# Performance work log

Hardware: AMD Instinct MI355X
Metric: run time of the kernel (lower is better)

Reference implementation:

```python
import jax, jax.numpy as jnp
import numpy as np

IOU_POS = 0.6
IOU_NEG = 0.45
BOX_W, CLS_W, INT_W = 1.0, 1.0, 0.5
ALPHA, GAMMA = 0.25, 2.0
BETA = 1.0 / 9.0
EPS = 1e-6


def setup_inputs() -> dict:
    key = jax.random.key(0)
    ks = jax.random.split(key, 8)
    B, N, M, C = 8, 131072, 48, 8
    cls_logits = jax.random.normal(ks[0], (B, N, 1), jnp.float32)
    box_preds = jax.random.normal(ks[1], (B, N, 6), jnp.float32) * 0.1
    intention_logits = jax.random.normal(ks[2], (B, N, C), jnp.float32)
    # anchors: 256x256 BEV grid over 100x100m, 2 orientations -> 131072 anchors
    side = int(np.sqrt(N // 2))
    xs = jnp.linspace(0.0, 100.0, side)
    gx, gy = jnp.meshgrid(xs, xs, indexing='ij')
    base = jnp.stack([gx.ravel(), gy.ravel()], axis=-1)  # [side^2, 2]
    n0 = side * side
    a0 = jnp.concatenate([base, jnp.full((n0, 1), 2.0), jnp.full((n0, 1), 4.5), jnp.zeros((n0, 1))], axis=-1)
    a1 = a0.at[:, 4].set(jnp.pi / 2)
    anchors = jnp.concatenate([a0, a1], axis=0)  # [N, 5] xywha
    gt_xy = jax.random.uniform(ks[3], (B, M, 2), minval=0.0, maxval=100.0)
    gt_w = jax.random.uniform(ks[4], (B, M, 1), minval=1.8, maxval=2.6)
    gt_l = jax.random.uniform(ks[5], (B, M, 1), minval=4.0, maxval=5.5)
    gt_a = jax.random.uniform(ks[6], (B, M, 1), minval=-jnp.pi, maxval=jnp.pi)
    gt_boxes = jnp.concatenate([gt_xy, gt_w, gt_l, gt_a], axis=-1)  # [B, M, 5]
    gt_intentions = jax.random.randint(ks[7], (B, M), 0, C, dtype=jnp.int32)
    return dict(cls_logits=cls_logits, box_preds=box_preds, intention_logits=intention_logits,
                anchors=anchors, gt_boxes=gt_boxes, gt_intentions=gt_intentions)


def _aa_iou(anchors, gt):
    # axis-aligned IoU on center-format boxes; anchors [N,5], gt [M,5] -> [N,M]
    ah = anchors[:, 2:4] * 0.5
    gh = gt[:, 2:4] * 0.5
    amin = anchors[:, None, :2] - ah[:, None]
    amax = anchors[:, None, :2] + ah[:, None]
    gmin = gt[None, :, :2] - gh[None]
    gmax = gt[None, :, :2] + gh[None]
    wh = jnp.clip(jnp.minimum(amax, gmax) - jnp.maximum(amin, gmin), 0.0)
    inter = wh[..., 0] * wh[..., 1]
    area_a = anchors[:, 2] * anchors[:, 3]
    area_g = gt[:, 2] * gt[:, 3]
    return inter / (area_a[:, None] + area_g[None, :] - inter + EPS)


def _assign(anchors, gt_b, gt_i):
    # single-sample target assignment; anchors [N,5], gt_b [M,5], gt_i [M]
    N = anchors.shape[0]
    M = gt_b.shape[0]
    iou = _aa_iou(anchors, gt_b)                       # [N, M]
    max_iou = iou.max(axis=1)                          # [N]
    argmax_gt = iou.argmax(axis=1)                     # [N]
    neg = max_iou < IOU_NEG
    pos = max_iou >= IOU_POS
    # force-match: best anchor per GT becomes positive if its IoU >= neg thresh
    force_idx = iou.argmax(axis=0)                     # [M]
    force_iou = iou[force_idx, jnp.arange(M)]          # [M]
    forced = jnp.zeros((N,), jnp.int32).at[force_idx].add((force_iou >= IOU_NEG).astype(jnp.int32)) > 0
    pos = pos | forced
    cls_t = jnp.where(pos, 1, jnp.where(neg, 0, -1))   # [N] in {-1,0,1}
    # box delta encode against the per-anchor best GT
    ag = gt_b[argmax_gt]                               # [N, 5]
    dx = (ag[:, 0] - anchors[:, 0]) / (anchors[:, 2] + EPS)
    dy = (ag[:, 1] - anchors[:, 1]) / (anchors[:, 3] + EPS)
    dw = jnp.log(ag[:, 2] / (anchors[:, 2] + EPS) + EPS)
    dl = jnp.log(ag[:, 3] / (anchors[:, 3] + EPS) + EPS)
    da = ag[:, 4] - anchors[:, 4]
    deltas = jnp.stack([dx, dy, dw, dl, jnp.sin(da), jnp.cos(da)], axis=1)  # [N,6]
    box_t = jnp.where(pos[:, None], deltas, 0.0)
    int_t = jnp.where(pos, gt_i[argmax_gt], -1)
    return cls_t, box_t, int_t


def reference(cls_logits, box_preds, intention_logits, anchors, gt_boxes, gt_intentions):
    cls_t, box_t, int_t = jax.vmap(_assign, in_axes=(None, 0, 0))(anchors, gt_boxes, gt_intentions)
    cls_t = cls_t.reshape(-1)
    box_t = box_t.reshape(-1, 6)
    int_t = int_t.reshape(-1)
    x = cls_logits.reshape(-1)
    bp = box_preds.reshape(-1, 6)
    il = intention_logits.reshape(-1, intention_logits.shape[-1])
    valid = cls_t >= 0
    pos = cls_t == 1
    num_pos = pos.sum()
    denom = jnp.maximum(1, num_pos).astype(jnp.float32)
    # sigmoid focal loss (sum over valid) / num_pos
    t = (cls_t == 1).astype(jnp.float32)
    ce = jnp.maximum(x, 0.0) - x * t + jnp.log1p(jnp.exp(-jnp.abs(x)))
    p = jax.nn.sigmoid(x)
    p_t = p * t + (1.0 - p) * (1.0 - t)
    alpha_t = ALPHA * t + (1.0 - ALPHA) * (1.0 - t)
    focal = alpha_t * ce * (1.0 - p_t) ** GAMMA
    cls_loss = jnp.where(valid, focal, 0.0).sum() / denom
    # smooth L1 (sum over positives) / num_pos
    d = jnp.abs(bp - box_t)
    sl1 = jnp.where(d < BETA, 0.5 * d * d / BETA, d - 0.5 * BETA)
    box_loss = jnp.where(pos[:, None], sl1, 0.0).sum() / denom
    # cross-entropy over positives / num_pos (no weights, no downsampling)
    logp = jax.nn.log_softmax(il, axis=-1)
    tgt = jnp.clip(int_t, 0, il.shape[-1] - 1)
    nll = -jnp.take_along_axis(logp, tgt[:, None], axis=1)[:, 0]
    intent_loss = jnp.where(pos, nll, 0.0).sum() / denom
    total = CLS_W * cls_loss + BOX_W * box_loss + INT_W * intent_loss
    return total, cls_loss, box_loss, intent_loss, num_pos.astype(jnp.float32)
```

## Files before the change

kernel.cpp:

```cpp
#include <hip/hip_runtime.h>
#include <cstddef>

#define IOU_POS_T 0.6f
#define IOU_NEG_T 0.45f
#define F_EPS 1e-6f
#define F_ALPHA 0.25f
#define F_BETA (1.0f/9.0f)
#define MAXM 64
#define PPB 512
#define BINF 3.402823466e+38f

__device__ __forceinline__ void fp_barrier(float& x) { asm volatile("" : "+v"(x)); }
__device__ __forceinline__ unsigned long long ullmax(unsigned long long a, unsigned long long b) {
    return a > b ? a : b;
}

__global__ void __launch_bounds__(256, 4)
dl_fused(const float* __restrict__ cls_logits, const float* __restrict__ box_preds,
         const float* __restrict__ intent_logits, const float* __restrict__ anchors,
         const float* __restrict__ gt_boxes, const int* __restrict__ gt_ints,
         float4* __restrict__ parts, int N, int M, int C, int nblkx)
{
    const int b = blockIdx.y;
    const int tid = threadIdx.x;
    const int blk = blockIdx.x;
    const int pbase = blk * PPB;
    const int half = N >> 1;
    const int wave = tid >> 6, lane = tid & 63;
    const int side = (int)sqrtf((float)half + 0.5f);
    const float step = 100.0f / (float)(side - 1);

    __shared__ float gmnx[MAXM], gmny[MAXM], gmxx[MAXM], gmxy[MAXM], gar[MAXM];
    __shared__ float gcx[MAXM], gcy[MAXM], gw[MAXM], gl[MAXM], ga[MAXM];
    __shared__ int gint[MAXM];
    __shared__ unsigned char sforce[PPB];
    __shared__ unsigned long long smask_s;
    __shared__ float q0[4], q1[4], q2[4], q3[4];

    float x0[2], x1[2];
    #pragma unroll
    for (int k = 0; k < 2; ++k) {
        const int p = pbase + k * 256 + tid;
        x0[k] = cls_logits[(size_t)b * N + p];
        x1[k] = cls_logits[(size_t)b * N + half + p];
    }

    if (tid < 64) {
        bool ov = false;
        if (tid < M) {
            const float* g = gt_boxes + ((size_t)b * M + tid) * 5;
            float cx = g[0], cy = g[1], w_ = g[2], l_ = g[3], ang = g[4];
            float hw = w_ * 0.5f, hl = l_ * 0.5f;
            float tmnx = cx - hw, tmxx = cx + hw;
            gmnx[tid] = tmnx; gmny[tid] = cy - hl;
            gmxx[tid] = tmxx; gmxy[tid] = cy + hl;
            gar[tid]  = w_ * l_;
            gcx[tid] = cx; gcy[tid] = cy; gw[tid] = w_; gl[tid] = l_; ga[tid] = ang;
            gint[tid] = gt_ints[(size_t)b * M + tid];
            float bmnx = (float)(2 * blk) * step - 1.0f - 0.01f;
            float bmxx = (float)(2 * blk + 1) * step + 1.0f + 0.01f;
            ov = (fminf(bmxx, tmxx) - fmaxf(bmnx, tmnx)) > 0.0f;
        }
        unsigned long long bal = __ballot(ov);
        if (tid == 0) smask_s = bal;
    }
    sforce[tid] = 0; sforce[tid + 256] = 0;
    __syncthreads();
    const unsigned long long sm = smask_s;

    float cls_acc = 0.0f, box_acc = 0.0f, int_acc = 0.0f, np_acc = 0.0f;

    if (sm == 0ull) {
        #pragma unroll
        for (int k = 0; k < 2; ++k) {
            {
                float x = x0[k];
                float ce = fmaxf(x, 0.0f) + log1pf(expf(-fabsf(x)));
                float pp = 1.0f / (1.0f + expf(-x));
                cls_acc += (1.0f - F_ALPHA) * ce * (pp * pp);
            }
            {
                float x = x1[k];
                float ce = fmaxf(x, 0.0f) + log1pf(expf(-fabsf(x)));
                float pp = 1.0f / (1.0f + expf(-x));
                cls_acc += (1.0f - F_ALPHA) * ce * (pp * pp);
            }
        }
    } else {
        {
            int j = 0;
            unsigned long long mm = sm;
            while (mm) {
                const int m = (int)__builtin_ctzll(mm); mm &= mm - 1;
                if ((j & 3) == wave) {
                    const float cxm = gcx[m], cym = gcy[m], gwm = gw[m], glm = gl[m];
                    const float gmnxm = gmnx[m], gmnym = gmny[m];
                    const float gmxxm = gmxx[m], gmxym = gmxy[m];
                    const float garea = gar[m];
                    const float hwx = (gwm + 2.0f) * 0.5f;
                    const float hwy = (glm + 4.5f) * 0.5f;
                    int gx0 = (int)floorf((cxm - hwx) / step) - 2; gx0 = gx0 < 0 ? 0 : gx0;
                    int gx1 = (int)ceilf ((cxm + hwx) / step) + 2; gx1 = gx1 > side-1 ? side-1 : gx1;
                    int gy0 = (int)floorf((cym - hwy) / step) - 2; gy0 = gy0 < 0 ? 0 : gy0;
                    int gy1 = (int)ceilf ((cym + hwy) / step) + 2; gy1 = gy1 > side-1 ? side-1 : gy1;
                    const int nyw = gy1 - gy0 + 1;
                    const int cnt = (gx1 - gx0 + 1) * nyw;
                    unsigned long long best = 0ull;
                    for (int idx = lane; idx < cnt; idx += 64) {
                        const int col = idx / nyw, row = idx - col * nyw;
                        const int i = (gx0 + col) * side + (gy0 + row);
                        const float* a = anchors + (size_t)i * 5;
                        float ax = a[0], ay = a[1], aw = a[2], al = a[3];
                        float amnx = ax - aw * 0.5f, amny = ay - al * 0.5f;
                        float amxx = ax + aw * 0.5f, amxy = ay + al * 0.5f;
                        float area_a = aw * al; fp_barrier(area_a);
                        float wx = fminf(amxx, gmxxm) - fmaxf(amnx, gmnxm); wx = fmaxf(wx, 0.0f);
                        float wy = fminf(amxy, gmxym) - fmaxf(amny, gmnym); wy = fmaxf(wy, 0.0f);
                        float inter = wx * wy; fp_barrier(inter);
                        if (inter > 0.0f) {
                            float denom = (area_a + garea) - inter + F_EPS;
                            float iou = inter / denom;
                            unsigned long long key =
                                ((unsigned long long)__float_as_uint(iou) << 32) | (unsigned)(~(unsigned)i);
                            best = ullmax(best, key);
                        }
                    }
                    #pragma unroll
                    for (int off = 32; off; off >>= 1)
                        best = ullmax(best, (unsigned long long)__shfl_down(best, off));
                    if (lane == 0) {
                        float fiou = __uint_as_float((unsigned)(best >> 32));
                        int fi = (int)(~(unsigned)best);
                        if (fiou >= IOU_NEG_T && fi >= pbase && fi < pbase + PPB)
                            sforce[fi - pbase] = 1;
                    }
                }
                ++j;
            }
        }
        float ax[2], ay[2], aw[2], al[2], aah0[2], aah1[2];
        #pragma unroll
        for (int k = 0; k < 2; ++k) {
            const int p = pbase + k * 256 + tid;
            const float* a = anchors + (size_t)p * 5;
            ax[k] = a[0]; ay[k] = a[1]; aw[k] = a[2]; al[k] = a[3]; aah0[k] = a[4];
            aah1[k] = anchors[(size_t)(p + half) * 5 + 4];
        }
        __syncthreads();

        #pragma unroll
        for (int k = 0; k < 2; ++k) {
            const int p = pbase + k * 256 + tid;
            const float amnx = ax[k] - aw[k] * 0.5f, amny = ay[k] - al[k] * 0.5f;
            const float amxx = ax[k] + aw[k] * 0.5f, amxy = ay[k] + al[k] * 0.5f;
            float area_a = aw[k] * al[k]; fp_barrier(area_a);
            unsigned long long mask = sm;
            float bestv = 0.0f; int bestm = 0;
            while (mask) {
                const int m = (int)__builtin_ctzll(mask); mask &= mask - 1;
                float wx = fminf(amxx, gmxx[m]) - fmaxf(amnx, gmnx[m]); wx = fmaxf(wx, 0.0f);
                float wy = fminf(amxy, gmxy[m]) - fmaxf(amny, gmny[m]); wy = fmaxf(wy, 0.0f);
                float inter = wx * wy; fp_barrier(inter);
                if (inter > 0.0f) {
                    float denom = (area_a + gar[m]) - inter + F_EPS;
                    float iou = inter / denom;
                    if (iou > bestv) { bestv = iou; bestm = m; }
                }
            }
            const bool neg = bestv < IOU_NEG_T;
            const bool forced = sforce[k * 256 + tid] != 0;
            const bool pos0 = (bestv >= IOU_POS_T) || forced;
            const bool pos1 = (bestv >= IOU_POS_T);
            const int m = bestm;

            float dx = 0, dy = 0, dwv = 0, dlv = 0;
            if (pos0 | pos1) {
                dx = (gcx[m] - ax[k]) / (aw[k] + F_EPS);
                dy = (gcy[m] - ay[k]) / (al[k] + F_EPS);
                dwv = logf(gw[m] / (aw[k] + F_EPS) + F_EPS);
                dlv = logf(gl[m] / (al[k] + F_EPS) + F_EPS);
            }
            if (pos0 || neg) {
                float x = x0[k];
                float t = pos0 ? 1.0f : 0.0f;
                float ce = fmaxf(x, 0.0f) - x * t + log1pf(expf(-fabsf(x)));
                float pp = 1.0f / (1.0f + expf(-x));
                float p_t = pp * t + (1.0f - pp) * (1.0f - t);
                float a_t = F_ALPHA * t + (1.0f - F_ALPHA) * (1.0f - t);
                float om = 1.0f - p_t;
                cls_acc += a_t * ce * (om * om);
            }
            if (pos0) {
                np_acc += 1.0f;
                float da = ga[m] - aah0[k];
                float tgt6[6] = { dx, dy, dwv, dlv, sinf(da), cosf(da) };
                const float* bp = box_preds + ((size_t)b * N + p) * 6;
                #pragma unroll
                for (int q = 0; q < 6; ++q) {
                    float d = fabsf(bp[q] - tgt6[q]);
                    box_acc += (d < F_BETA) ? (0.5f * d * d / F_BETA) : (d - 0.5f * F_BETA);
                }
                const float* il = intent_logits + ((size_t)b * N + p) * C;
                float mx = il[0];
                for (int c = 1; c < C; ++c) mx = fmaxf(mx, il[c]);
                float se = 0.0f;
                for (int c = 0; c < C; ++c) se += expf(il[c] - mx);
                int tg = gint[m]; tg = tg < 0 ? 0 : (tg > C - 1 ? C - 1 : tg);
                int_acc += (mx + logf(se)) - il[tg];
            }
            if (pos1 || neg) {
                float x = x1[k];
                float t = pos1 ? 1.0f : 0.0f;
                float ce = fmaxf(x, 0.0f) - x * t + log1pf(expf(-fabsf(x)));
                float pp = 1.0f / (1.0f + expf(-x));
                float p_t = pp * t + (1.0f - pp) * (1.0f - t);
                float a_t = F_ALPHA * t + (1.0f - F_ALPHA) * (1.0f - t);
                float om = 1.0f - p_t;
                cls_acc += a_t * ce * (om * om);
            }
            if (pos1) {
                np_acc += 1.0f;
                const int i1 = p + half;
                float da = ga[m] - aah1[k];
                float tgt6[6] = { dx, dy, dwv, dlv, sinf(da), cosf(da) };
                const float* bp = box_preds + ((size_t)b * N + i1) * 6;
                #pragma unroll
                for (int q = 0; q < 6; ++q) {
                    float d = fabsf(bp[q] - tgt6[q]);
                    box_acc += (d < F_BETA) ? (0.5f * d * d / F_BETA) : (d - 0.5f * F_BETA);
                }
                const float* il = intent_logits + ((size_t)b * N + i1) * C;
                float mx = il[0];
                for (int c = 1; c < C; ++c) mx = fmaxf(mx, il[c]);
                float se = 0.0f;
                for (int c = 0; c < C; ++c) se += expf(il[c] - mx);
                int tg = gint[m]; tg = tg < 0 ? 0 : (tg > C - 1 ? C - 1 : tg);
                int_acc += (mx + logf(se)) - il[tg];
            }
        }
    }

    #pragma unroll
    for (int off = 32; off; off >>= 1) {
        cls_acc += __shfl_down(cls_acc, off);
        box_acc += __shfl_down(box_acc, off);
        int_acc += __shfl_down(int_acc, off);
        np_acc  += __shfl_down(np_acc, off);
    }
    if ((tid & 63) == 0) { q0[wave] = cls_acc; q1[wave] = box_acc; q2[wave] = int_acc; q3[wave] = np_acc; }
    __syncthreads();
    if (tid == 0) {
        parts[(size_t)b * nblkx + blk] =
            make_float4(q0[0] + q0[1] + q0[2] + q0[3],
                        q1[0] + q1[1] + q1[2] + q1[3],
                        q2[0] + q2[1] + q2[2] + q2[3],
                        q3[0] + q3[1] + q3[2] + q3[3]);
    }
}

__global__ void __launch_bounds__(256)
dl_reduce(const float4* __restrict__ parts, int total, float* __restrict__ out)
{
    const int tid = threadIdx.x;
    float c = 0, bx = 0, it = 0, np = 0;
    for (int k = tid; k < total; k += 256) {
        float4 v = parts[k];
        c += v.x; bx += v.y; it += v.z; np += v.w;
    }
    #pragma unroll
    for (int off = 32; off; off >>= 1) {
        c  += __shfl_down(c, off);
        bx += __shfl_down(bx, off);
        it += __shfl_down(it, off);
        np += __shfl_down(np, off);
    }
    __shared__ float q0[4], q1[4], q2[4], q3[4];
    const int wave = tid >> 6;
    if ((tid & 63) == 0) { q0[wave] = c; q1[wave] = bx; q2[wave] = it; q3[wave] = np; }
    __syncthreads();
    if (tid == 0) {
        float cs = q0[0] + q0[1] + q0[2] + q0[3];
        float bs = q1[0] + q1[1] + q1[2] + q1[3];
        float is = q2[0] + q2[1] + q2[2] + q2[3];
        float ns = q3[0] + q3[1] + q3[2] + q3[3];
        float denom = fmaxf(1.0f, ns);
        float cls = cs / denom, bo = bs / denom, in_ = is / denom;
        out[0] = cls + bo + 0.5f * in_;
        out[1] = cls;
        out[2] = bo;
        out[3] = in_;
        out[4] = ns;
    }
}

extern "C" void kernel_launch(void* const* d_in, const int* in_sizes, int n_in,
                              void* d_out, int out_size, void* d_ws, size_t ws_size,
                              hipStream_t stream) {
    const float* cls_logits    = (const float*)d_in[0];
    const float* box_preds     = (const float*)d_in[1];
    const float* intent_logits = (const float*)d_in[2];
    const float* anchors       = (const float*)d_in[3];
    const float* gt_boxes      = (const float*)d_in[4];
    const int*   gt_ints       = (const int*)d_in[5];

    const int N = in_sizes[3] / 5;
    const int B = in_sizes[0] / N;
    const int M = in_sizes[5] / B;
    const int C = in_sizes[2] / in_sizes[0];
    const int half = N / 2;
    const int nblkx = (half + PPB - 1) / PPB;

    float4* parts = (float4*)d_ws;

    dim3 grid(nblkx, B);
    dl_fused<<<grid, 256, 0, stream>>>(cls_logits, box_preds, intent_logits, anchors,
                                       gt_boxes, gt_ints, parts, N, M, C, nblkx);
    dl_reduce<<<1, 256, 0, stream>>>(parts, nblkx * B, (float*)d_out);
}
```

Baseline: 32.05 us.

## Double anchors per block and load four contiguous logits per thread as float4

Each block now covers 1024 anchor positions (4 BEV grid columns) instead of 512, and each thread handles 4 contiguous positions loaded with float4 vector loads rather than strided scalar loads. The GT overlap culling window widens to match, and the per-block setup (GT staging, ballot, force-match scan) is amortized over more anchors with half as many blocks. The risks are fewer blocks to fill the GPU, more blocks that cannot take the no-GT fast path because of the wider window, and more registers per thread. The parts of the kernel not shown, such as the block-count computation and the reduction, must match the new PPB.

```diff
diff --git a/kernel.cpp b/kernel.cpp
--- a/kernel.cpp
+++ b/kernel.cpp
@@ -7,7 +7,7 @@
 #define F_ALPHA 0.25f
 #define F_BETA (1.0f/9.0f)
 #define MAXM 64
-#define PPB 512
+#define PPB 1024
 #define BINF 3.402823466e+38f
 
 __device__ __forceinline__ void fp_barrier(float& x) { asm volatile("" : "+v"(x)); }
@@ -29,6 +29,7 @@
     const int wave = tid >> 6, lane = tid & 63;
     const int side = (int)sqrtf((float)half + 0.5f);
     const float step = 100.0f / (float)(side - 1);
+    const int p4 = pbase + 4 * tid;
 
     __shared__ float gmnx[MAXM], gmny[MAXM], gmxx[MAXM], gmxy[MAXM], gar[MAXM];
     __shared__ float gcx[MAXM], gcy[MAXM], gw[MAXM], gl[MAXM], ga[MAXM];
@@ -37,12 +38,22 @@
     __shared__ unsigned long long smask_s;
     __shared__ float q0[4], q1[4], q2[4], q3[4];
 
-    float x0[2], x1[2];
-    #pragma unroll
-    for (int k = 0; k < 2; ++k) {
-        const int p = pbase + k * 256 + tid;
-        x0[k] = cls_logits[(size_t)b * N + p];
-        x1[k] = cls_logits[(size_t)b * N + half + p];
+    float xs0[4], xs1[4];
+    {
+        const bool ok = (p4 + 3) < half;
+        if (ok) {
+            float4 v0 = *reinterpret_cast<const float4*>(&cls_logits[(size_t)b * N + p4]);
+            float4 v1 = *reinterpret_cast<const float4*>(&cls_logits[(size_t)b * N + half + p4]);
+            xs0[0] = v0.x; xs0[1] = v0.y; xs0[2] = v0.z; xs0[3] = v0.w;
+            xs1[0] = v1.x; xs1[1] = v1.y; xs1[2] = v1.z; xs1[3] = v1.w;
+        } else {
+            #pragma unroll
+            for (int k = 0; k < 4; ++k) {
+                const int p = p4 + k;
+                xs0[k] = (p < half) ? cls_logits[(size_t)b * N + p] : 0.0f;
+                xs1[k] = (p < half) ? cls_logits[(size_t)b * N + half + p] : 0.0f;
+            }
+        }
     }
 
     if (tid < 64) {
@@ -57,14 +68,14 @@
             gar[tid]  = w_ * l_;
             gcx[tid] = cx; gcy[tid] = cy; gw[tid] = w_; gl[tid] = l_; ga[tid] = ang;
             gint[tid] = gt_ints[(size_t)b * M + tid];
-            float bmnx = (float)(2 * blk) * step - 1.0f - 0.01f;
-            float bmxx = (float)(2 * blk + 1) * step + 1.0f + 0.01f;
+            float bmnx = (float)(4 * blk) * step - 1.0f - 0.01f;
+            float bmxx = (float)(4 * blk + 3) * step + 1.0f + 0.01f;
             ov = (fminf(bmxx, tmxx) - fmaxf(bmnx, tmnx)) > 0.0f;
         }
         unsigned long long bal = __ballot(ov);
         if (tid == 0) smask_s = bal;
     }
-    sforce[tid] = 0; sforce[tid + 256] = 0;
+    sforce[tid] = 0; sforce[tid + 256] = 0; sforce[tid + 512] = 0; sforce[tid + 768] = 0;
     __syncthreads();
     const unsigned long long sm = smask_s;
 
@@ -72,15 +83,15 @@
 
     if (sm == 0ull) {
         #pragma unroll
-        for (int k = 0; k < 2; ++k) {
+        for (int k = 0; k < 4; ++k) {
             {
-                float x = x0[k];
+                float x = xs0[k];
                 float ce = fmaxf(x, 0.0f) + log1pf(expf(-fabsf(x)));
                 float pp = 1.0f / (1.0f + expf(-x));
                 cls_acc += (1.0f - F_ALPHA) * ce * (pp * pp);
             }
             {
-                float x = x1[k];
+                float x = xs1[k];
                 float ce = fmaxf(x, 0.0f) + log1pf(expf(-fabsf(x)));
                 float pp = 1.0f / (1.0f + expf(-x));
                 cls_acc += (1.0f - F_ALPHA) * ce * (pp * pp);
@@ -138,19 +149,24 @@
                 ++j;
             }
         }
-        float ax[2], ay[2], aw[2], al[2], aah0[2], aah1[2];
+        float ax[4], ay[4], aw[4], al[4], aah0[4], aah1[4];
         #pragma unroll
-        for (int k = 0; k < 2; ++k) {
-            const int p = pbase + k * 256 + tid;
-            const float* a = anchors + (size_t)p * 5;
-            ax[k] = a[0]; ay[k] = a[1]; aw[k] = a[2]; al[k] = a[3]; aah0[k] = a[4];
-            aah1[k] = anchors[(size_t)(p + half) * 5 + 4];
+        for (int k = 0; k < 4; ++k) {
+            const int p = p4 + k;
+            if (p < half) {
+                const float* a = anchors + (size_t)p * 5;
+                ax[k] = a[0]; ay[k] = a[1]; aw[k] = a[2]; al[k] = a[3]; aah0[k] = a[4];
+                aah1[k] = anchors[(size_t)(p + half) * 5 + 4];
+            } else {
+                ax[k] = 0; ay[k] = 0; aw[k] = 0; al[k] = 0; aah0[k] = 0; aah1[k] = 0;
+            }
         }
         __syncthreads();
 
         #pragma unroll
-        for (int k = 0; k < 2; ++k) {
-            const int p = pbase + k * 256 + tid;
+        for (int k = 0; k < 4; ++k) {
+            const int p = p4 + k;
+            if (p >= half) continue;
             const float amnx = ax[k] - aw[k] * 0.5f, amny = ay[k] - al[k] * 0.5f;
             const float amxx = ax[k] + aw[k] * 0.5f, amxy = ay[k] + al[k] * 0.5f;
             float area_a = aw[k] * al[k]; fp_barrier(area_a);
@@ -168,7 +184,7 @@
                 }
             }
             const bool neg = bestv < IOU_NEG_T;
-            const bool forced = sforce[k * 256 + tid] != 0;
+            const bool forced = sforce[p - pbase] != 0;
             const bool pos0 = (bestv >= IOU_POS_T) || forced;
             const bool pos1 = (bestv >= IOU_POS_T);
             const int m = bestm;
@@ -181,7 +197,7 @@
                 dlv = logf(gl[m] / (al[k] + F_EPS) + F_EPS);
             }
             if (pos0 || neg) {
-                float x = x0[k];
+                float x = xs0[k];
                 float t = pos0 ? 1.0f : 0.0f;
                 float ce = fmaxf(x, 0.0f) - x * t + log1pf(expf(-fabsf(x)));
                 float pp = 1.0f / (1.0f + expf(-x));
@@ -209,7 +225,7 @@
                 int_acc += (mx + logf(se)) - il[tg];
             }
             if (pos1 || neg) {
-                float x = x1[k];
+                float x = xs1[k];
                 float t = pos1 ? 1.0f : 0.0f;
                 float ce = fmaxf(x, 0.0f) - x * t + log1pf(expf(-fabsf(x)));
                 float pp = 1.0f / (1.0f + expf(-x));
```

New measurement: 44.40 us. 1.39x slower.
